# Optimization experiments

Measured on AMD Instinct MI355X. Metric: run time of the kernel, lower is better.

The kernel has to match this reference:

```python
import jax, jax.numpy as jnp
import numpy as np

D_MODEL = 1024
NUM_HEADS = 16
D_K = D_MODEL // NUM_HEADS  # 64
THETA = 10000.0


def apply_rope(t, positions):
    # t: [b, h, s, d], positions: [s] int
    d = t.shape[-1]
    inv_freq = 1.0 / (THETA ** (jnp.arange(0, d, 2, dtype=jnp.float32) / d))  # [d/2]
    ang = positions.astype(jnp.float32)[:, None] * inv_freq[None, :]  # [s, d/2]
    cos = jnp.cos(ang)[None, None]  # [1,1,s,d/2]
    sin = jnp.sin(ang)[None, None]
    x1 = t[..., 0::2]
    x2 = t[..., 1::2]
    r1 = x1 * cos - x2 * sin
    r2 = x1 * sin + x2 * cos
    # interleave back: [..., d/2, 2] -> [..., d]
    return jnp.stack([r1, r2], axis=-1).reshape(t.shape)


def setup_inputs() -> dict:
    key = jax.random.key(0)
    ks = jax.random.split(key, 5)
    b, s = 4, 2048
    scale = 1.0 / np.sqrt(D_MODEL)
    return {
        "x": jax.random.normal(ks[0], (b, s, D_MODEL), dtype=jnp.float32),
        "Wq": jax.random.normal(ks[1], (D_MODEL, D_MODEL), dtype=jnp.float32) * scale,
        "Wk": jax.random.normal(ks[2], (D_MODEL, D_MODEL), dtype=jnp.float32) * scale,
        "Wv": jax.random.normal(ks[3], (D_MODEL, D_MODEL), dtype=jnp.float32) * scale,
        "Wo": jax.random.normal(ks[4], (D_MODEL, D_MODEL), dtype=jnp.float32) * scale,
        "token_positions": jnp.arange(s, dtype=jnp.int32),
    }


def reference(x, Wq, Wk, Wv, Wo, token_positions):
    b, s, _ = x.shape
    # nn.Linear with no bias: y = x @ W.T
    def proj(W):
        y = jnp.einsum('bsd,ed->bse', x, W)
        return y.reshape(b, s, NUM_HEADS, D_K).transpose(0, 2, 1, 3)  # [b,h,s,dk]
    Q = apply_rope(proj(Wq), token_positions)
    K = apply_rope(proj(Wk), token_positions)
    V = proj(Wv)
    scores = jnp.einsum('bhqd,bhkd->bhqk', Q, K) / np.sqrt(D_K).astype(np.float32)
    causal = jnp.arange(s)[:, None] >= jnp.arange(s)[None, :]  # [s,s] lower-tri True
    scores = jnp.where(causal[None, None], scores, -jnp.inf)
    probs = jax.nn.softmax(scores, axis=-1)
    out = jnp.einsum('bhqk,bhkd->bhqd', probs, V)  # [b,h,s,dk]
    out = out.transpose(0, 2, 1, 3).reshape(b, s, D_MODEL)
    return jnp.einsum('bsd,ed->bse', out, Wo)
```

## Files before the change

### kernel.cpp

```cpp
#include <hip/hip_runtime.h>
#include <stdint.h>

#define SLEN 2048
#define DMODEL 1024
#define NHEADS 16
#define MTOT 8192

typedef short s16x8 __attribute__((ext_vector_type(8)));
typedef short s16x4 __attribute__((ext_vector_type(4)));
typedef float f32x4 __attribute__((ext_vector_type(4)));
typedef float f32x16 __attribute__((ext_vector_type(16)));
typedef unsigned u32x2 __attribute__((ext_vector_type(2)));
typedef unsigned u32x4 __attribute__((ext_vector_type(4)));

static __device__ __forceinline__ unsigned short f2bf(float f) {
  unsigned u = __builtin_bit_cast(unsigned, f);
  u += 0x7fffu + ((u >> 16) & 1u);
  return (unsigned short)(u >> 16);
}

static __device__ __forceinline__ unsigned cvt_pk_bf16(float lo, float hi) {
  unsigned r;
  asm("v_cvt_pk_bf16_f32 %0, %1, %2" : "=v"(r) : "v"(lo), "v"(hi));
  return r;
}

static __device__ __forceinline__ void gload_lds16(const void* g, void* l) {
  __builtin_amdgcn_global_load_lds((__attribute__((address_space(1))) void*)g,
                                   (__attribute__((address_space(3))) void*)l,
                                   16, 0, 0);
}

#define EXP2R(x) __builtin_amdgcn_exp2f(x)

#define MFMA16(a, b, c) __builtin_amdgcn_mfma_f32_16x16x32_bf16(a, b, c, 0, 0, 0)
#define MFMA32(a, b, c) __builtin_amdgcn_mfma_f32_32x32x16_bf16(a, b, c, 0, 0, 0)
#define SWZ(r) ((((r) & 7) ^ (((r) >> 3) & 7)))

__global__ void __launch_bounds__(256) rope_table(const int* __restrict__ pos,
                                                  float* __restrict__ ctab,
                                                  float* __restrict__ stab) {
  int g = blockIdx.x * 256 + threadIdx.x;
  int s = g >> 5, i = g & 31;
  float p = (float)pos[s];
  float ang = p * exp2f(-(float)i * 0.41524101186092029f);
  ctab[g] = cosf(ang);
  stab[g] = sinf(ang);
}

__global__ void __launch_bounds__(256) cvt_f32_bf16(const float* __restrict__ src,
                                                    unsigned short* __restrict__ dst,
                                                    int n8) {
  int i = blockIdx.x * 256 + threadIdx.x;
  if (i >= n8) return;
  f32x4 a = ((const f32x4*)src)[i * 2];
  f32x4 b = ((const f32x4*)src)[i * 2 + 1];
  s16x8 o;
#pragma unroll
  for (int j = 0; j < 4; ++j) o[j] = (short)f2bf(a[j]);
#pragma unroll
  for (int j = 0; j < 4; ++j) o[4 + j] = (short)f2bf(b[j]);
  ((s16x8*)dst)[i] = o;
}

__global__ void __launch_bounds__(256) cvt_weights(const float* __restrict__ w0,
                                                   const float* __restrict__ w1,
                                                   const float* __restrict__ w2,
                                                   const float* __restrict__ w3,
                                                   unsigned short* __restrict__ d0,
                                                   unsigned short* __restrict__ d1,
                                                   unsigned short* __restrict__ d2,
                                                   unsigned short* __restrict__ d3) {
  int which = blockIdx.y;
  const float* src = which == 0 ? w0 : which == 1 ? w1 : which == 2 ? w2 : w3;
  unsigned short* dst = which == 0 ? d0 : which == 1 ? d1 : which == 2 ? d2 : d3;
  int i = blockIdx.x * 256 + threadIdx.x;
  f32x4 a = ((const f32x4*)src)[i * 2];
  f32x4 b = ((const f32x4*)src)[i * 2 + 1];
  s16x8 o;
#pragma unroll
  for (int j = 0; j < 4; ++j) o[j] = (short)f2bf(a[j]);
#pragma unroll
  for (int j = 0; j < 4; ++j) o[4 + j] = (short)f2bf(b[j]);
  ((s16x8*)dst)[i] = o;
}

template<int MODE>
__global__ void __launch_bounds__(256) gemm_nt(const unsigned short* __restrict__ A,
                                               const unsigned short* __restrict__ B,
                                               void* __restrict__ dstQ,
                                               void* __restrict__ dstK,
                                               void* __restrict__ dstV,
                                               const float* __restrict__ ctab,
                                               const float* __restrict__ stab,
                                               float scale) {
  __shared__ unsigned short ldsA[3][128 * 32];
  __shared__ unsigned short ldsB[3][128 * 32];
  const int tid = threadIdx.x;
  const int lane = tid & 63;
  const int wave = tid >> 6;
  const int wm = wave >> 1, wn = wave & 1;

  int m0, n0;
  if constexpr (MODE == 3) {
    int flat = blockIdx.y * 24 + blockIdx.x;
    int xcd = flat & 7, idx = flat >> 3;
    int g = idx >> 6;
    int local = idx & 63;
    int lm = local >> 3, ln = local & 7;
    m0 = (xcd * 8 + lm) * 128;
    n0 = (g * 8 + ln) * 128;
  } else {
    int flat = blockIdx.y * 8 + blockIdx.x;
    int logical = (flat & 7) * 64 + (flat >> 3);
    m0 = (logical >> 3) * 128;
    n0 = (logical & 7) * 128;
  }
  const int l15 = lane & 15, lhi = lane >> 4;

  f32x4 acc[4][4] = {};

  auto stage = [&](int buf, int kt) {
    const int kbase = kt * 32;
#pragma unroll
    for (int issue = 0; issue < 2; ++issue) {
      int c = issue * 256 + wave * 64 + lane;
      int row = c >> 2, kc = c & 3;
      int kcg = kc ^ ((row >> 1) & 3);
      gload_lds16(A + (size_t)(m0 + row) * 1024 + kbase + kcg * 8,
                  &ldsA[buf][(issue * 256 + wave * 64) * 8]);
      gload_lds16(B + (size_t)(n0 + row) * 1024 + kbase + kcg * 8,
                  &ldsB[buf][(issue * 256 + wave * 64) * 8]);
    }
  };

  stage(0, 0);
  stage(1, 1);
  for (int kt = 0; kt < 32; ++kt) {
    if (kt + 1 < 32) {
      asm volatile("s_waitcnt vmcnt(4)" ::: "memory");
    } else {
      asm volatile("s_waitcnt vmcnt(0)" ::: "memory");
    }
    __builtin_amdgcn_s_barrier();
    __builtin_amdgcn_sched_barrier(0);
    if (kt + 2 < 32) stage((kt + 2) % 3, kt + 2);

    const int buf = kt % 3;
    s16x8 af[4], bf[4];
#pragma unroll
    for (int mi = 0; mi < 4; ++mi) {
      int row = wm * 64 + mi * 16 + l15;
      int kc = lhi ^ ((row >> 1) & 3);
      af[mi] = *(const s16x8*)&ldsA[buf][row * 32 + kc * 8];
    }
#pragma unroll
    for (int ni = 0; ni < 4; ++ni) {
      int row = wn * 64 + ni * 16 + l15;
      int kc = lhi ^ ((row >> 1) & 3);
      bf[ni] = *(const s16x8*)&ldsB[buf][row * 32 + kc * 8];
    }
#pragma unroll
    for (int mi = 0; mi < 4; ++mi)
#pragma unroll
      for (int ni = 0; ni < 4; ++ni)
        acc[mi][ni] = MFMA16(af[mi], bf[ni], acc[mi][ni]);
  }

  if constexpr (MODE == 0) {
    float* dst = (float*)dstQ;
#pragma unroll
    for (int mi = 0; mi < 4; ++mi)
#pragma unroll
      for (int ni = 0; ni < 4; ++ni)
#pragma unroll
        for (int i = 0; i < 4; ++i) {
          int r = m0 + wm * 64 + mi * 16 + lhi * 4 + i;
          int n = n0 + wn * 64 + ni * 16 + l15;
          dst[(size_t)r * 1024 + n] = acc[mi][ni][i];
        }
  } else {
    const int which = n0 >> 10;
    if (which < 2) {
      unsigned short* dst = (unsigned short*)(which == 0 ? dstQ : dstK);
      const float sc = (which == 0) ? scale : 1.0f;
#pragma unroll
      for (int mi = 0; mi < 4; ++mi)
#pragma unroll
        for (int ni = 0; ni < 4; ++ni)
#pragma unroll
          for (int i = 0; i < 4; ++i) {
            int r = m0 + wm * 64 + mi * 16 + lhi * 4 + i;
            int nn = (n0 & 1023) + wn * 64 + ni * 16 + l15;
            float v = acc[mi][ni][i];
            float p = __shfl_xor(v, 1);
            int s = r & (SLEN - 1);
            int d = nn & 63;
            int fi = d >> 1;
            float c = ctab[s * 32 + fi], sn = stab[s * 32 + fi];
            float o = (d & 1) ? (p * sn + v * c) : (v * c - p * sn);
            o *= sc;
            int b = r >> 11, h = nn >> 6;
            dst[((size_t)(b * NHEADS + h) * SLEN + s) * 64 + d] = f2bf(o);
          }
    } else {
      unsigned short* dst = (unsigned short*)dstV;
#pragma unroll
      for (int mi = 0; mi < 4; ++mi)
#pragma unroll
        for (int ni = 0; ni < 4; ++ni) {
          int r0 = m0 + wm * 64 + mi * 16 + lhi * 4;
          int nn = (n0 & 1023) + wn * 64 + ni * 16 + l15;
          int b = r0 >> 11, s0 = r0 & (SLEN - 1);
          int h = nn >> 6, d = nn & 63;
          s16x4 pk;
#pragma unroll
          for (int i = 0; i < 4; ++i) pk[i] = (short)f2bf(acc[mi][ni][i]);
          *(s16x4*)&dst[((size_t)(b * NHEADS + h) * 64 + d) * SLEN + s0] = pk;
        }
    }
  }
}

__global__ void __launch_bounds__(256, 4) flash_attn(const unsigned short* __restrict__ Q,
                                                     const unsigned short* __restrict__ K,
                                                     const unsigned short* __restrict__ Vt,
                                                     unsigned short* __restrict__ Obf) {
  __shared__ unsigned short Kbuf[2][64 * 64];
  __shared__ unsigned short Vbuf[2][64 * 64];

  const int tid = threadIdx.x, lane = tid & 63, w = tid >> 6;
  const int l31 = lane & 31, h = lane >> 5;

  int id = blockIdx.x;
  int xcd = id & 7, idx = id >> 3;
  const int s_ = idx & 3;
  const int bhl = (idx >> 2) & 7;
  const int g_ = idx >> 5;
  const int mul2g = (g_ == 0) ? 0 : (g_ == 1) ? 2 : (g_ == 2) ? 3 : 1;
  const int t = 4 * (s_ ^ g_) + (s_ ^ mul2g);
  const int bh = xcd * 8 + bhl;
  const int b = bh >> 4, hd = bh & 15;

  const unsigned short* Qb = Q + (size_t)bh * SLEN * 64;
  const unsigned short* Kb = K + (size_t)bh * SLEN * 64;
  const unsigned short* Vb = Vt + (size_t)bh * 64 * SLEN;

  const int qbase = t * 128;
  const int nt = 2 * t + 2;
  const int q_abs = qbase + w * 32 + l31;
  const int qminw = qbase + w * 32;

  auto stageKV = [&](int buf, int k0) {
#pragma unroll
    for (int i = 0; i < 2; ++i) {
      int c = i * 256 + tid;
      int row = c >> 3, cg = c & 7;
      int col = ((cg ^ SWZ(row)) * 8);
      gload_lds16(Kb + (size_t)(k0 + row) * 64 + col, &Kbuf[buf][c * 8]);
      gload_lds16(Vb + (size_t)row * SLEN + k0 + col, &Vbuf[buf][c * 8]);
    }
  };

  s16x8 qf[4];
#pragma unroll
  for (int dc = 0; dc < 4; ++dc)
    qf[dc] = *(const s16x8*)&Qb[(size_t)q_abs * 64 + dc * 16 + h * 8];

  f32x16 accT[2] = {};
  float m_run = -3.0e38f, l_run = 0.f;

  stageKV(0, 0);
  for (int kt = 0; kt < nt; ++kt) {
    const int cur = kt & 1;
    const int k0 = kt * 64;
    asm volatile("s_waitcnt vmcnt(0)" ::: "memory");
    __builtin_amdgcn_s_barrier();
    __builtin_amdgcn_sched_barrier(0);
    if (kt + 1 < nt) stageKV(cur ^ 1, (kt + 1) * 64);

    {
      f32x16 sacc[2] = {};
      __builtin_amdgcn_s_setprio(1);
#pragma unroll
      for (int kb = 0; kb < 2; ++kb) {
#pragma unroll
        for (int dc = 0; dc < 4; ++dc) {
          int r = kb * 32 + l31;
          int g = dc * 2 + h;
          s16x8 kf = *(const s16x8*)&Kbuf[cur][r * 64 + ((g ^ SWZ(r)) * 8)];
          sacc[kb] = MFMA32(kf, qf[dc], sacc[kb]);
        }
      }
      __builtin_amdgcn_s_setprio(0);

      if (k0 + 63 > qminw) {
#pragma unroll
        for (int kb = 0; kb < 2; ++kb)
#pragma unroll
          for (int r = 0; r < 16; ++r) {
            int k_abs = k0 + kb * 32 + (r & 3) + 8 * (r >> 2) + 4 * h;
            if (k_abs > q_abs) sacc[kb][r] = -3.0e38f;
          }
      }

      float p0 = fmaxf(sacc[0][0], sacc[1][0]);
      float p1 = fmaxf(sacc[0][1], sacc[1][1]);
      float p2 = fmaxf(sacc[0][2], sacc[1][2]);
      float p3 = fmaxf(sacc[0][3], sacc[1][3]);
#pragma unroll
      for (int r = 4; r < 16; r += 4) {
        p0 = fmaxf(p0, fmaxf(sacc[0][r + 0], sacc[1][r + 0]));
        p1 = fmaxf(p1, fmaxf(sacc[0][r + 1], sacc[1][r + 1]));
        p2 = fmaxf(p2, fmaxf(sacc[0][r + 2], sacc[1][r + 2]));
        p3 = fmaxf(p3, fmaxf(sacc[0][r + 3], sacc[1][r + 3]));
      }
      float mx = fmaxf(fmaxf(p0, p1), fmaxf(p2, p3));
      mx = fmaxf(mx, __shfl_xor(mx, 32));

      if (!__all(mx <= m_run)) {
        float mnew = fmaxf(m_run, mx);
        float facv = EXP2R(m_run - mnew);
        m_run = mnew;
        l_run *= facv;
#pragma unroll
        for (int db = 0; db < 2; ++db)
#pragma unroll
          for (int r = 0; r < 16; ++r) accT[db][r] *= facv;
      }

      float s0 = 0.f, s1 = 0.f, s2 = 0.f, s3 = 0.f;
#pragma unroll
      for (int kb = 0; kb < 2; ++kb)
#pragma unroll
        for (int r = 0; r < 16; r += 4) {
          float e0 = EXP2R(sacc[kb][r + 0] - m_run);
          float e1 = EXP2R(sacc[kb][r + 1] - m_run);
          float e2 = EXP2R(sacc[kb][r + 2] - m_run);
          float e3 = EXP2R(sacc[kb][r + 3] - m_run);
          sacc[kb][r + 0] = e0; sacc[kb][r + 1] = e1;
          sacc[kb][r + 2] = e2; sacc[kb][r + 3] = e3;
          s0 += e0; s1 += e1; s2 += e2; s3 += e3;
        }
      float sum = (s0 + s1) + (s2 + s3);
      sum += __shfl_xor(sum, 32);
      l_run += sum;

      unsigned Hv[8][2];
#pragma unroll
      for (int kb = 0; kb < 2; ++kb)
#pragma unroll
        for (int q4 = 0; q4 < 4; ++q4) {
          Hv[kb * 4 + q4][0] = cvt_pk_bf16(sacc[kb][q4 * 4 + 0], sacc[kb][q4 * 4 + 1]);
          Hv[kb * 4 + q4][1] = cvt_pk_bf16(sacc[kb][q4 * 4 + 2], sacc[kb][q4 * 4 + 3]);
        }

      __builtin_amdgcn_s_setprio(1);
#pragma unroll
      for (int db = 0; db < 2; ++db) {
        int r = db * 32 + l31;
        const char* rowp = (const char*)&Vbuf[cur][r * 64];
#pragma unroll
        for (int kc = 0; kc < 4; ++kc) {
          u32x2 vlo = *(const u32x2*)(rowp + (((2 * kc) ^ SWZ(r)) * 16) + 8 * h);
          u32x2 vhi = *(const u32x2*)(rowp + (((2 * kc + 1) ^ SWZ(r)) * 16) + 8 * h);
          u32x4 vv;
          vv[0] = vlo[0]; vv[1] = vlo[1]; vv[2] = vhi[0]; vv[3] = vhi[1];
          u32x4 pv;
          pv[0] = Hv[2 * kc][0]; pv[1] = Hv[2 * kc][1];
          pv[2] = Hv[2 * kc + 1][0]; pv[3] = Hv[2 * kc + 1][1];
          accT[db] = MFMA32(__builtin_bit_cast(s16x8, vv),
                            __builtin_bit_cast(s16x8, pv), accT[db]);
        }
      }
      __builtin_amdgcn_s_setprio(0);
    }
  }

  float linv = 1.f / l_run;
#pragma unroll
  for (int db = 0; db < 2; ++db)
#pragma unroll
    for (int q4 = 0; q4 < 4; ++q4) {
      u32x2 pk;
      pk[0] = cvt_pk_bf16(accT[db][q4 * 4 + 0] * linv, accT[db][q4 * 4 + 1] * linv);
      pk[1] = cvt_pk_bf16(accT[db][q4 * 4 + 2] * linv, accT[db][q4 * 4 + 3] * linv);
      int d0 = db * 32 + 8 * q4 + 4 * h;
      *(u32x2*)&Obf[((size_t)(b * SLEN + q_abs)) * DMODEL + hd * 64 + d0] = pk;
    }
}

extern "C" void kernel_launch(void* const* d_in, const int* in_sizes, int n_in,
                              void* d_out, int out_size, void* d_ws, size_t ws_size,
                              hipStream_t stream) {
  const float* x  = (const float*)d_in[0];
  const float* Wq = (const float*)d_in[1];
  const float* Wk = (const float*)d_in[2];
  const float* Wv = (const float*)d_in[3];
  const float* Wo = (const float*)d_in[4];
  const int* pos  = (const int*)d_in[5];
  float* out = (float*)d_out;

  char* ws = (char*)d_ws;
  size_t off = 0;
  auto take = [&](size_t bytes) {
    char* p = ws + off;
    off += (bytes + 255) & ~(size_t)255;
    return p;
  };
  unsigned short* xbf  = (unsigned short*)take((size_t)MTOT * DMODEL * 2);
  unsigned short* wqkv = (unsigned short*)take((size_t)3 * DMODEL * DMODEL * 2);
  unsigned short* wobf = (unsigned short*)take((size_t)DMODEL * DMODEL * 2);
  unsigned short* Qs   = (unsigned short*)take((size_t)64 * SLEN * 64 * 2);
  unsigned short* Ks   = (unsigned short*)take((size_t)64 * SLEN * 64 * 2);
  unsigned short* Vt   = (unsigned short*)take((size_t)64 * 64 * SLEN * 2);
  unsigned short* Obf  = (unsigned short*)take((size_t)MTOT * DMODEL * 2);
  float* ctab = (float*)take((size_t)SLEN * 32 * 4);
  float* stab = (float*)take((size_t)SLEN * 32 * 4);

  rope_table<<<256, 256, 0, stream>>>(pos, ctab, stab);
  cvt_f32_bf16<<<4096, 256, 0, stream>>>(x, xbf, MTOT * DMODEL / 8);
  cvt_weights<<<dim3(512, 4), 256, 0, stream>>>(
      Wq, Wk, Wv, Wo,
      wqkv, wqkv + (size_t)DMODEL * DMODEL, wqkv + (size_t)2 * DMODEL * DMODEL, wobf);

  gemm_nt<3><<<dim3(24, 64), 256, 0, stream>>>(xbf, wqkv, Qs, Ks, Vt,
                                               ctab, stab, 0.18033688011112042f);

  flash_attn<<<1024, 256, 0, stream>>>(Qs, Ks, Vt, Obf);

  gemm_nt<0><<<dim3(8, 64), 256, 0, stream>>>(Obf, wobf, out, nullptr, nullptr,
                                              nullptr, nullptr, 1.0f);
}
```

Measured before the change: 178.2 us.

## Fuse prep kernels, enlarge GEMM tiles to 256x128, add lazy softmax rescale

Merges the rope table and the three bf16 conversion kernels into one launch to cut launch overhead. The projection GEMMs move to 512-thread blocks with 256x128 tiles and a K-step of 64, double-buffered instead of triple-buffered with a full vmcnt(0) wait, aiming for more reuse per LDS load. Flash attention now skips the running-max rescale unless the max grows by more than 8, which saves exp and multiply work but allows larger intermediate values. The full wait may expose load latency, and the larger LDS footprint may reduce occupancy.

```diff
diff --git a/kernel.cpp b/kernel.cpp
--- a/kernel.cpp
+++ b/kernel.cpp
@@ -37,134 +37,134 @@
 #define MFMA32(a, b, c) __builtin_amdgcn_mfma_f32_32x32x16_bf16(a, b, c, 0, 0, 0)
 #define SWZ(r) ((((r) & 7) ^ (((r) >> 3) & 7)))
 
-__global__ void __launch_bounds__(256) rope_table(const int* __restrict__ pos,
-                                                  float* __restrict__ ctab,
-                                                  float* __restrict__ stab) {
-  int g = blockIdx.x * 256 + threadIdx.x;
-  int s = g >> 5, i = g & 31;
-  float p = (float)pos[s];
-  float ang = p * exp2f(-(float)i * 0.41524101186092029f);
-  ctab[g] = cosf(ang);
-  stab[g] = sinf(ang);
-}
-
-__global__ void __launch_bounds__(256) cvt_f32_bf16(const float* __restrict__ src,
-                                                    unsigned short* __restrict__ dst,
-                                                    int n8) {
-  int i = blockIdx.x * 256 + threadIdx.x;
-  if (i >= n8) return;
-  f32x4 a = ((const f32x4*)src)[i * 2];
-  f32x4 b = ((const f32x4*)src)[i * 2 + 1];
-  s16x8 o;
-#pragma unroll
-  for (int j = 0; j < 4; ++j) o[j] = (short)f2bf(a[j]);
-#pragma unroll
-  for (int j = 0; j < 4; ++j) o[4 + j] = (short)f2bf(b[j]);
-  ((s16x8*)dst)[i] = o;
-}
-
-__global__ void __launch_bounds__(256) cvt_weights(const float* __restrict__ w0,
-                                                   const float* __restrict__ w1,
-                                                   const float* __restrict__ w2,
-                                                   const float* __restrict__ w3,
-                                                   unsigned short* __restrict__ d0,
-                                                   unsigned short* __restrict__ d1,
-                                                   unsigned short* __restrict__ d2,
-                                                   unsigned short* __restrict__ d3) {
-  int which = blockIdx.y;
-  const float* src = which == 0 ? w0 : which == 1 ? w1 : which == 2 ? w2 : w3;
-  unsigned short* dst = which == 0 ? d0 : which == 1 ? d1 : which == 2 ? d2 : d3;
-  int i = blockIdx.x * 256 + threadIdx.x;
-  f32x4 a = ((const f32x4*)src)[i * 2];
-  f32x4 b = ((const f32x4*)src)[i * 2 + 1];
-  s16x8 o;
-#pragma unroll
-  for (int j = 0; j < 4; ++j) o[j] = (short)f2bf(a[j]);
-#pragma unroll
-  for (int j = 0; j < 4; ++j) o[4 + j] = (short)f2bf(b[j]);
-  ((s16x8*)dst)[i] = o;
+__global__ void __launch_bounds__(256) prep(const float* __restrict__ x,
+                                            const float* __restrict__ Wq,
+                                            const float* __restrict__ Wk,
+                                            const float* __restrict__ Wv,
+                                            const float* __restrict__ Wo,
+                                            const int* __restrict__ pos,
+                                            unsigned short* __restrict__ xbf,
+                                            unsigned short* __restrict__ wqkv,
+                                            unsigned short* __restrict__ wobf,
+                                            float* __restrict__ ctab,
+                                            float* __restrict__ stab) {
+  int blk = blockIdx.x;
+  if (blk < 4096) {
+    int i = blk * 256 + threadIdx.x;
+    f32x4 a = ((const f32x4*)x)[i * 2];
+    f32x4 b = ((const f32x4*)x)[i * 2 + 1];
+    s16x8 o;
+#pragma unroll
+    for (int j = 0; j < 4; ++j) o[j] = (short)f2bf(a[j]);
+#pragma unroll
+    for (int j = 0; j < 4; ++j) o[4 + j] = (short)f2bf(b[j]);
+    ((s16x8*)xbf)[i] = o;
+  } else if (blk < 6144) {
+    int wsel = (blk - 4096) >> 9;
+    const float* src = wsel == 0 ? Wq : wsel == 1 ? Wk : wsel == 2 ? Wv : Wo;
+    unsigned short* dst = (wsel < 3) ? (wqkv + (size_t)wsel * DMODEL * DMODEL) : wobf;
+    int i = ((blk - 4096) & 511) * 256 + threadIdx.x;
+    f32x4 a = ((const f32x4*)src)[i * 2];
+    f32x4 b = ((const f32x4*)src)[i * 2 + 1];
+    s16x8 o;
+#pragma unroll
+    for (int j = 0; j < 4; ++j) o[j] = (short)f2bf(a[j]);
+#pragma unroll
+    for (int j = 0; j < 4; ++j) o[4 + j] = (short)f2bf(b[j]);
+    ((s16x8*)dst)[i] = o;
+  } else {
+    int g = (blk - 6144) * 256 + threadIdx.x;
+    int s = g >> 5, i = g & 31;
+    float p = (float)pos[s];
+    float ang = p * exp2f(-(float)i * 0.41524101186092029f);
+    ctab[g] = cosf(ang);
+    stab[g] = sinf(ang);
+  }
 }
 
 template<int MODE>
-__global__ void __launch_bounds__(256) gemm_nt(const unsigned short* __restrict__ A,
-                                               const unsigned short* __restrict__ B,
-                                               void* __restrict__ dstQ,
-                                               void* __restrict__ dstK,
-                                               void* __restrict__ dstV,
-                                               const float* __restrict__ ctab,
-                                               const float* __restrict__ stab,
-                                               float scale) {
-  __shared__ unsigned short ldsA[3][128 * 32];
-  __shared__ unsigned short ldsB[3][128 * 32];
+__global__ void __launch_bounds__(512, 2) gemm256(const unsigned short* __restrict__ A,
+                                                  const unsigned short* __restrict__ B,
+                                                  void* __restrict__ dstQ,
+                                                  void* __restrict__ dstK,
+                                                  void* __restrict__ dstV,
+                                                  const float* __restrict__ ctab,
+                                                  const float* __restrict__ stab,
+                                                  float scale) {
+  __shared__ unsigned short ldsA[2][256 * 64];
+  __shared__ unsigned short ldsB[2][128 * 64];
   const int tid = threadIdx.x;
   const int lane = tid & 63;
   const int wave = tid >> 6;
   const int wm = wave >> 1, wn = wave & 1;
+  const int l15 = lane & 15, lhi = lane >> 4;
 
   int m0, n0;
   if constexpr (MODE == 3) {
     int flat = blockIdx.y * 24 + blockIdx.x;
     int xcd = flat & 7, idx = flat >> 3;
-    int g = idx >> 6;
-    int local = idx & 63;
+    int g = idx >> 5;
+    int local = idx & 31;
     int lm = local >> 3, ln = local & 7;
-    m0 = (xcd * 8 + lm) * 128;
+    m0 = (xcd * 4 + lm) * 256;
     n0 = (g * 8 + ln) * 128;
   } else {
-    int flat = blockIdx.y * 8 + blockIdx.x;
-    int logical = (flat & 7) * 64 + (flat >> 3);
-    m0 = (logical >> 3) * 128;
-    n0 = (logical & 7) * 128;
+    int flat = blockIdx.x;
+    int xcd = flat & 7, idx = flat >> 3;
+    int lm = idx >> 3, ln = idx & 7;
+    m0 = (xcd * 4 + lm) * 256;
+    n0 = ln * 128;
   }
-  const int l15 = lane & 15, lhi = lane >> 4;
 
   f32x4 acc[4][4] = {};
 
   auto stage = [&](int buf, int kt) {
-    const int kbase = kt * 32;
-#pragma unroll
-    for (int issue = 0; issue < 2; ++issue) {
-      int c = issue * 256 + wave * 64 + lane;
-      int row = c >> 2, kc = c & 3;
-      int kcg = kc ^ ((row >> 1) & 3);
-      gload_lds16(A + (size_t)(m0 + row) * 1024 + kbase + kcg * 8,
-                  &ldsA[buf][(issue * 256 + wave * 64) * 8]);
-      gload_lds16(B + (size_t)(n0 + row) * 1024 + kbase + kcg * 8,
-                  &ldsB[buf][(issue * 256 + wave * 64) * 8]);
+    const int kbase = kt * 64;
+#pragma unroll
+    for (int i = 0; i < 4; ++i) {
+      int c = i * 512 + tid;
+      int row = c >> 3, cg = c & 7;
+      gload_lds16(A + (size_t)(m0 + row) * 1024 + kbase + ((cg ^ (row & 7)) * 8),
+                  &ldsA[buf][c * 8]);
+    }
+#pragma unroll
+    for (int i = 0; i < 2; ++i) {
+      int c = i * 512 + tid;
+      int row = c >> 3, cg = c & 7;
+      gload_lds16(B + (size_t)(n0 + row) * 1024 + kbase + ((cg ^ (row & 7)) * 8),
+                  &ldsB[buf][c * 8]);
     }
   };
 
   stage(0, 0);
-  stage(1, 1);
-  for (int kt = 0; kt < 32; ++kt) {
-    if (kt + 1 < 32) {
-      asm volatile("s_waitcnt vmcnt(4)" ::: "memory");
-    } else {
-      asm volatile("s_waitcnt vmcnt(0)" ::: "memory");
-    }
+  for (int kt = 0; kt < 16; ++kt) {
+    const int cur = kt & 1;
+    asm volatile("s_waitcnt vmcnt(0)" ::: "memory");
     __builtin_amdgcn_s_barrier();
     __builtin_amdgcn_sched_barrier(0);
-    if (kt + 2 < 32) stage((kt + 2) % 3, kt + 2);
-
-    const int buf = kt % 3;
-    s16x8 af[4], bf[4];
-#pragma unroll
-    for (int mi = 0; mi < 4; ++mi) {
-      int row = wm * 64 + mi * 16 + l15;
-      int kc = lhi ^ ((row >> 1) & 3);
-      af[mi] = *(const s16x8*)&ldsA[buf][row * 32 + kc * 8];
-    }
-#pragma unroll
-    for (int ni = 0; ni < 4; ++ni) {
-      int row = wn * 64 + ni * 16 + l15;
-      int kc = lhi ^ ((row >> 1) & 3);
-      bf[ni] = *(const s16x8*)&ldsB[buf][row * 32 + kc * 8];
-    }
-#pragma unroll
-    for (int mi = 0; mi < 4; ++mi)
-#pragma unroll
-      for (int ni = 0; ni < 4; ++ni)
-        acc[mi][ni] = MFMA16(af[mi], bf[ni], acc[mi][ni]);
+    if (kt + 1 < 16) stage(cur ^ 1, kt + 1);
+
+    s16x8 af[4][2], bf[4][2];
+#pragma unroll
+    for (int kk = 0; kk < 2; ++kk) {
+#pragma unroll
+      for (int mi = 0; mi < 4; ++mi) {
+        int row = wm * 64 + mi * 16 + l15;
+        af[mi][kk] = *(const s16x8*)&ldsA[cur][row * 64 + (((kk * 4 + lhi) ^ (row & 7)) * 8)];
+      }
+#pragma unroll
+      for (int ni = 0; ni < 4; ++ni) {
+        int row = wn * 64 + ni * 16 + l15;
+        bf[ni][kk] = *(const s16x8*)&ldsB[cur][row * 64 + (((kk * 4 + lhi) ^ (row & 7)) * 8)];
+      }
+    }
+#pragma unroll
+    for (int kk = 0; kk < 2; ++kk)
+#pragma unroll
+      for (int mi = 0; mi < 4; ++mi)
+#pragma unroll
+        for (int ni = 0; ni < 4; ++ni)
+          acc[mi][ni] = MFMA16(af[mi][kk], bf[ni][kk], acc[mi][ni]);
   }
 
   if constexpr (MODE == 0) {
@@ -318,7 +318,7 @@
       float mx = fmaxf(fmaxf(p0, p1), fmaxf(p2, p3));
       mx = fmaxf(mx, __shfl_xor(mx, 32));
 
-      if (!__all(mx <= m_run)) {
+      if (!__all(mx - m_run <= 8.0f)) {
         float mnew = fmaxf(m_run, mx);
         float facv = EXP2R(m_run - mnew);
         m_run = mnew;
@@ -418,17 +418,14 @@
   float* ctab = (float*)take((size_t)SLEN * 32 * 4);
   float* stab = (float*)take((size_t)SLEN * 32 * 4);
 
-  rope_table<<<256, 256, 0, stream>>>(pos, ctab, stab);
-  cvt_f32_bf16<<<4096, 256, 0, stream>>>(x, xbf, MTOT * DMODEL / 8);
-  cvt_weights<<<dim3(512, 4), 256, 0, stream>>>(
-      Wq, Wk, Wv, Wo,
-      wqkv, wqkv + (size_t)DMODEL * DMODEL, wqkv + (size_t)2 * DMODEL * DMODEL, wobf);
-
-  gemm_nt<3><<<dim3(24, 64), 256, 0, stream>>>(xbf, wqkv, Qs, Ks, Vt,
+  prep<<<6400, 256, 0, stream>>>(x, Wq, Wk, Wv, Wo, pos,
+                                 xbf, wqkv, wobf, ctab, stab);
+
+  gemm256<3><<<dim3(24, 32), 512, 0, stream>>>(xbf, wqkv, Qs, Ks, Vt,
                                                ctab, stab, 0.18033688011112042f);
 
   flash_attn<<<1024, 256, 0, stream>>>(Qs, Ks, Vt, Obf);
 
-  gemm_nt<0><<<dim3(8, 64), 256, 0, stream>>>(Obf, wobf, out, nullptr, nullptr,
-                                              nullptr, nullptr, 1.0f);
-}
+  gemm256<0><<<256, 512, 0, stream>>>(Obf, wobf, out, nullptr, nullptr,
+                                      nullptr, nullptr, 1.0f);
+}
```

Measured after the change: 176.1 us. About the same (-1.2%).
